# Optimization experiments

Hardware: AMD Instinct MI355X
Metric: run time of the kernel (lower is better)

The kernel has to match this reference:

```python
import jax, jax.numpy as jnp
import numpy as np

P = 5            # assets (fixed by 5x5 MLP)
K = 4            # stacked layers
LB, UB = 0.0, 0.5
RF = 1.03
B = 524288       # batch size
ALPHA, OMEGA, BETA, MU = 0.1, 0.05, 0.05, 0.01
MAX_REBAL_ITERS = 8  # water-filling clamp loop converges in a few iters for P=5


def setup_inputs() -> dict:
    key = jax.random.key(0)
    k1, k2, k3, k4 = jax.random.split(key, 4)
    x1 = jax.random.uniform(k1, (B,), dtype=jnp.float32)                 # wealth per sample
    x2 = jax.random.uniform(k2, (B, P, P), dtype=jnp.float32)            # prev covariance
    eps = jax.random.normal(k3, (K, B, P), dtype=jnp.float32)            # N(0,I) draw per layer
    W = jax.random.normal(k4, (K, 3, P, P), dtype=jnp.float32) * 0.5     # 3 bias-free Linear(5,5) per layer
    return {"x1": x1, "x2": x2, "eps": eps, "W": W}


def _rebalance(w):
    """Vectorized clamp/redistribute loop over the whole batch. w: (B,P)."""
    old = w
    new = jnp.clip(w, LB, UB)
    done = jnp.zeros(w.shape[0], dtype=bool)

    def body(carry, _):
        old, new, done = carry
        leftover = jnp.sum(old - new, axis=1, keepdims=True)            # (B,1)
        masked = jnp.where(new != UB, new, 0.0)                          # non-capped weights
        new2 = new + leftover * masked / jnp.sum(masked, axis=1, keepdims=True)
        cont = jnp.any(new2 > UB, axis=1)                                # (B,)
        new3 = jnp.where(cont[:, None], jnp.clip(new2, LB, UB), new2)
        # freeze rows that already converged
        old_n = jnp.where(done[:, None], old, new2)
        new_n = jnp.where(done[:, None], new, new3)
        return (old_n, new_n, done | ~cont), None

    (_, new, _), _ = jax.lax.scan(body, (old, new, done), None, length=MAX_REBAL_ITERS)
    return new


def reference(x1, x2, eps, W):
    # Replicates the original bug: every StackLayer consumes the ORIGINAL
    # (x1, x2); only the last layer's output is returned.
    for k in range(K):
        Ce = jnp.einsum('bij,bj->bi', x2, eps[k])                        # prev_cov @ eps, (B,P)
        curr_cov = OMEGA + ALPHA * x2 + BETA * (Ce ** 2)[:, None, :]     # (B,P,P), row-broadcast
        R = MU + Ce                                                      # (B,P)
        h = R
        for l in range(3):                                               # torch Linear: x @ W.T
            h = jnp.tanh(h @ W[k, l].T)
        wts = jax.nn.softmax(h, axis=1)
        wts = _rebalance(wts)
        wealth = jnp.sum(x1[:, None] * wts * (1.0 + R) * RF, axis=1)     # (B,)
    return wealth, curr_cov
```

## Files before the change

### kernel.cpp

```cpp
#include <hip/hip_runtime.h>
#include <cmath>

#define P 5
#define LBV 0.0f
#define UBV 0.5f
#define RFV 1.03f
#define ALPHA 0.1f
#define OMEGA 0.05f
#define BETA 0.05f
#define MU 0.01f
#define NTHR 256

#define AS1 __attribute__((address_space(1)))
#define AS3 __attribute__((address_space(3)))

__device__ __forceinline__ float fast_tanh(float x) {
    float ax = fabsf(x);
    float t  = __expf(-2.0f * ax);
    float r  = (1.0f - t) * __builtin_amdgcn_rcpf(1.0f + t);
    return copysignf(r, x);
}

__global__ __launch_bounds__(NTHR, 5) void portfolio_kernel(
    const float* __restrict__ x1,
    const float* __restrict__ x2,
    const float* __restrict__ eps,
    const float* __restrict__ W,
    float* __restrict__ out, int B)
{
    __shared__ float sX2[NTHR * P * P];

    const int tid  = threadIdx.x;
    const int b0   = blockIdx.x * NTHR;
    const int lane = tid & 63;
    const int wv   = tid >> 6;

    float x1v = x1[b0 + tid];
    const float* ge = eps + (size_t)3 * B * P + (size_t)(b0 + tid) * P;
    float e[P];
    #pragma unroll
    for (int j = 0; j < P; ++j) e[j] = ge[j];

    const float* gx2 = x2 + (size_t)b0 * (P * P);
    #pragma unroll
    for (int i = 0; i < 6; ++i) {
        int c = (i * 4 + wv) * 256;
        __builtin_amdgcn_global_load_lds((const AS1 void*)(gx2 + c + lane * 4),
                                         (AS3 void*)(&sX2[c]), 16, 0, 0);
    }
    if (wv == 0) {
        __builtin_amdgcn_global_load_lds((const AS1 void*)(gx2 + 6144 + lane * 4),
                                         (AS3 void*)(&sX2[6144]), 16, 0, 0);
    }
    __syncthreads();

    float r2[P * P];
    #pragma unroll
    for (int i = 0; i < P * P; ++i) r2[i] = sX2[tid * (P * P) + i];

    float Ce[P];
    #pragma unroll
    for (int i = 0; i < P; ++i) {
        float s = 0.0f;
        #pragma unroll
        for (int j = 0; j < P; ++j) s = fmaf(r2[i * P + j], e[j], s);
        Ce[i] = s;
    }

    float R[P], h[P];
    #pragma unroll
    for (int i = 0; i < P; ++i) { R[i] = MU + Ce[i]; h[i] = R[i]; }

    const float* Wl = W + 3 * 3 * P * P;
    #pragma unroll
    for (int l = 0; l < 3; ++l) {
        float hn[P];
        #pragma unroll
        for (int i = 0; i < P; ++i) {
            float s = 0.0f;
            #pragma unroll
            for (int j = 0; j < P; ++j) s = fmaf(h[j], Wl[l * P * P + i * P + j], s);
            hn[i] = fast_tanh(s);
        }
        #pragma unroll
        for (int i = 0; i < P; ++i) h[i] = hn[i];
    }

    float w[P], ssum = 0.0f;
    #pragma unroll
    for (int i = 0; i < P; ++i) { w[i] = __expf(h[i]); ssum += w[i]; }
    float rs = __builtin_amdgcn_rcpf(ssum);
    #pragma unroll
    for (int i = 0; i < P; ++i) w[i] *= rs;

    float oldv[P], nw[P];
    #pragma unroll
    for (int i = 0; i < P; ++i) {
        oldv[i] = w[i];
        nw[i]   = fminf(fmaxf(w[i], LBV), UBV);
    }
    #pragma unroll
    for (int it = 0; it < 8; ++it) {
        float leftover = 0.0f;
        #pragma unroll
        for (int i = 0; i < P; ++i) leftover += oldv[i] - nw[i];
        float mk[P], msum = 0.0f;
        #pragma unroll
        for (int i = 0; i < P; ++i) {
            mk[i] = (nw[i] != UBV) ? nw[i] : 0.0f;
            msum += mk[i];
        }
        float scale = leftover * __builtin_amdgcn_rcpf(msum);
        float n2[P];
        #pragma unroll
        for (int i = 0; i < P; ++i) n2[i] = fmaf(scale, mk[i], nw[i]);
        bool cont = false;
        #pragma unroll
        for (int i = 0; i < P; ++i) cont = cont || (n2[i] > UBV);
        #pragma unroll
        for (int i = 0; i < P; ++i) {
            oldv[i] = n2[i];
            nw[i]   = cont ? fminf(fmaxf(n2[i], LBV), UBV) : n2[i];
        }
        if (!cont) break;
    }

    float ws = 0.0f;
    #pragma unroll
    for (int i = 0; i < P; ++i) ws = fmaf(nw[i], 1.0f + R[i], ws);
    out[b0 + tid] = x1v * ws * RFV;

    float ce2[P];
    #pragma unroll
    for (int j = 0; j < P; ++j) ce2[j] = Ce[j] * Ce[j];
    float* gout = out + B + (size_t)(b0 + tid) * (P * P);
    #pragma unroll
    for (int i = 0; i < P; ++i) {
        #pragma unroll
        for (int j = 0; j < P; ++j)
            gout[i * P + j] = fmaf(BETA, ce2[j], fmaf(ALPHA, r2[i * P + j], OMEGA));
    }
}

extern "C" void kernel_launch(void* const* d_in, const int* in_sizes, int n_in,
                              void* d_out, int out_size, void* d_ws, size_t ws_size,
                              hipStream_t stream) {
    const float* x1  = (const float*)d_in[0];
    const float* x2  = (const float*)d_in[1];
    const float* eps = (const float*)d_in[2];
    const float* W   = (const float*)d_in[3];
    float* out = (float*)d_out;
    const int B = in_sizes[0];
    const int blocks = B / NTHR;
    portfolio_kernel<<<blocks, NTHR, 0, stream>>>(x1, x2, eps, W, out, B);
}
```

Baseline: 142.5 us.

## Use per-wave LDS staging for x2, eps loads and coalesced covariance stores

Each wavefront now stages its own 64-sample slice of x2 and eps into LDS with direct global-to-LDS loads and waits only on its own vmcnt, so the block-wide __syncthreads is gone. The strided per-thread eps loads become coalesced. The 25-float covariance output is written back into LDS and then stored to global memory as coalesced float4 writes instead of strided per-thread scalar stores. This relies on a hand-coded waitcnt immediate and wave-local LDS visibility, which is fragile. It also uses a little more LDS per block.

After: 136.1 us. 1.05x faster.

```diff
diff --git a/kernel.cpp b/kernel.cpp
--- a/kernel.cpp
+++ b/kernel.cpp
@@ -28,35 +28,43 @@
     const float* __restrict__ W,
     float* __restrict__ out, int B)
 {
-    __shared__ float sX2[NTHR * P * P];
+    __shared__ alignas(16) float sX2[4 * 1600];
+    __shared__ alignas(16) float sE[4 * 320];
 
     const int tid  = threadIdx.x;
-    const int b0   = blockIdx.x * NTHR;
     const int lane = tid & 63;
     const int wv   = tid >> 6;
+    const int bw   = blockIdx.x * NTHR + wv * 64;
 
-    float x1v = x1[b0 + tid];
-    const float* ge = eps + (size_t)3 * B * P + (size_t)(b0 + tid) * P;
-    float e[P];
+    float x1v = x1[bw + lane];
+
+    const float* gx2  = x2 + (size_t)bw * (P * P);
+    float*       ldsx = &sX2[wv * 1600];
     #pragma unroll
-    for (int j = 0; j < P; ++j) e[j] = ge[j];
+    for (int i = 0; i < 6; ++i)
+        __builtin_amdgcn_global_load_lds((const AS1 void*)(gx2 + i * 256 + lane * 4),
+                                         (AS3 void*)(ldsx + i * 256), 16, 0, 0);
+    __builtin_amdgcn_global_load_lds((const AS1 void*)(gx2 + 1536 + lane),
+                                     (AS3 void*)(ldsx + 1536), 4, 0, 0);
 
-    const float* gx2 = x2 + (size_t)b0 * (P * P);
-    #pragma unroll
-    for (int i = 0; i < 6; ++i) {
-        int c = (i * 4 + wv) * 256;
-        __builtin_amdgcn_global_load_lds((const AS1 void*)(gx2 + c + lane * 4),
-                                         (AS3 void*)(&sX2[c]), 16, 0, 0);
-    }
-    if (wv == 0) {
-        __builtin_amdgcn_global_load_lds((const AS1 void*)(gx2 + 6144 + lane * 4),
-                                         (AS3 void*)(&sX2[6144]), 16, 0, 0);
-    }
-    __syncthreads();
+    const float* ge   = eps + (size_t)3 * B * P + (size_t)bw * P;
+    float*       ldse = &sE[wv * 320];
+    __builtin_amdgcn_global_load_lds((const AS1 void*)(ge + lane * 4),
+                                     (AS3 void*)(ldse), 16, 0, 0);
+    __builtin_amdgcn_global_load_lds((const AS1 void*)(ge + 256 + lane),
+                                     (AS3 void*)(ldse + 256), 4, 0, 0);
+
+    __builtin_amdgcn_sched_barrier(0);
+    __builtin_amdgcn_s_waitcnt(0x0F70);
+    __builtin_amdgcn_sched_barrier(0);
 
     float r2[P * P];
     #pragma unroll
-    for (int i = 0; i < P * P; ++i) r2[i] = sX2[tid * (P * P) + i];
+    for (int i = 0; i < P * P; ++i) r2[i] = ldsx[lane * (P * P) + i];
+
+    float e[P];
+    #pragma unroll
+    for (int j = 0; j < P; ++j) e[j] = ldse[lane * P + j];
 
     float Ce[P];
     #pragma unroll
@@ -128,18 +136,26 @@
     float ws = 0.0f;
     #pragma unroll
     for (int i = 0; i < P; ++i) ws = fmaf(nw[i], 1.0f + R[i], ws);
-    out[b0 + tid] = x1v * ws * RFV;
+    out[bw + lane] = x1v * ws * RFV;
 
     float ce2[P];
     #pragma unroll
     for (int j = 0; j < P; ++j) ce2[j] = Ce[j] * Ce[j];
-    float* gout = out + B + (size_t)(b0 + tid) * (P * P);
     #pragma unroll
     for (int i = 0; i < P; ++i) {
         #pragma unroll
         for (int j = 0; j < P; ++j)
-            gout[i * P + j] = fmaf(BETA, ce2[j], fmaf(ALPHA, r2[i * P + j], OMEGA));
+            ldsx[lane * (P * P) + i * P + j] =
+                fmaf(BETA, ce2[j], fmaf(ALPHA, r2[i * P + j], OMEGA));
     }
+
+    float* gout = out + B + (size_t)bw * (P * P);
+    const float4* s4 = (const float4*)ldsx;
+    float4* g4 = (float4*)gout;
+    #pragma unroll
+    for (int r = 0; r < 6; ++r)
+        g4[r * 64 + lane] = s4[r * 64 + lane];
+    gout[1536 + lane] = ldsx[1536 + lane];
 }
 
 extern "C" void kernel_launch(void* const* d_in, const int* in_sizes, int n_in,
```
